# Kernel tuning notes

Hardware: AMD Instinct MI355X
Metric: run time of the kernel (lower is better)

## Reference

```python
import jax, jax.numpy as jnp
import numpy as np

N, DIM, K = 65536, 512, 256


def setup_inputs() -> dict:
    key = jax.random.key(0)
    k1, k2 = jax.random.split(key)
    embeddings = jax.random.normal(k1, (N, DIM), dtype=jnp.float32)
    # Centroid table produced by the (external, non-differentiable) faiss
    # k-means fit; materialized here as a learned parameter.
    centroids = jax.random.normal(k2, (K, DIM), dtype=jnp.float32)
    return {"embeddings": embeddings, "centroids": centroids, "batch_id": 0}


def reference(embeddings, centroids, batch_id):
    # Batched equivalent of the Python loop over samples:
    # for each embedding, cdist to centroids, take the 2nd-nearest centroid.
    # Squared L2 preserves the ordering of torch.cdist (monotone sqrt),
    # and the output is a gather of centroids, so math is identical.
    # d2: [N, K]
    d2 = (
        jnp.sum(embeddings * embeddings, axis=1, keepdims=True)
        - 2.0 * jnp.einsum("nd,kd->nk", embeddings, centroids)
        + jnp.sum(centroids * centroids, axis=1)
    )
    # top-2 smallest distances -> indices of nearest and 2nd-nearest centroids
    _, top2_idx = jax.lax.top_k(-d2, 2)  # [N, 2]
    hard_neg_idx = top2_idx[:, 1]  # second-nearest centroid per sample
    return centroids[hard_neg_idx]  # [N, DIM]
```

## Files before the change

### kernel.cpp

```cpp
#include <hip/hip_runtime.h>

#define N_EMB 65536
#define DIM   512
#define K_C   256
#define NCHUNK (DIM / 32)
#define RPW   16
#define WAVES 4
#define THETA 1.5f


typedef __attribute__((ext_vector_type(4))) float        f32x4;
typedef __attribute__((ext_vector_type(8))) __bf16       bf16x8;
typedef __attribute__((ext_vector_type(8))) short        s16x8;
typedef __attribute__((ext_vector_type(4))) unsigned int u32x4;

template <class T>
__device__ inline auto mfma_bf16_t(T a, T b, f32x4 c, int)
    -> decltype(__builtin_amdgcn_mfma_f32_16x16x32_bf16(a, b, c, 0, 0, 0)) {
  return __builtin_amdgcn_mfma_f32_16x16x32_bf16(a, b, c, 0, 0, 0);
}
template <class T>
__device__ inline f32x4 mfma_bf16_t(T a, T b, f32x4 c, long) {
  return __builtin_amdgcn_mfma_f32_16x16x32_bf16(
      __builtin_bit_cast(s16x8, a), __builtin_bit_cast(s16x8, b), c, 0, 0, 0);
}
__device__ inline f32x4 MFMA(bf16x8 a, bf16x8 b, f32x4 c) {
  return mfma_bf16_t(a, b, c, 0);
}

__device__ inline unsigned umin_(unsigned a, unsigned b) { return a < b ? a : b; }
__device__ inline unsigned umax_(unsigned a, unsigned b) { return a > b ? a : b; }

__device__ inline u32x4 pack8hi(const float4 a, const float4 b) {
  return (u32x4){
      (__float_as_uint(a.x) >> 16) | (__float_as_uint(a.y) & 0xFFFF0000u),
      (__float_as_uint(a.z) >> 16) | (__float_as_uint(a.w) & 0xFFFF0000u),
      (__float_as_uint(b.x) >> 16) | (__float_as_uint(b.y) & 0xFFFF0000u),
      (__float_as_uint(b.z) >> 16) | (__float_as_uint(b.w) & 0xFFFF0000u)};
}

__device__ inline u32x4 cvt8hi_rne(const float4 a, const float4 b) {
  float v[8] = {a.x, a.y, a.z, a.w, b.x, b.y, b.z, b.w};
  unsigned h[8];
#pragma unroll
  for (int i = 0; i < 8; ++i) {
    const unsigned u = __float_as_uint(v[i]);
    h[i] = (u + 0x7FFFu + ((u >> 16) & 1u)) >> 16;
  }
  return (u32x4){h[0] | (h[1] << 16), h[2] | (h[3] << 16),
                 h[4] | (h[5] << 16), h[6] | (h[7] << 16)};
}

__global__ void pack_centroids(const float* __restrict__ cent,
                               unsigned* __restrict__ cbh,
                               float* __restrict__ cnorm) {
  const int k    = blockIdx.x;
  const int lane = threadIdx.x;
  const float* src = cent + (size_t)k * DIM + lane * 8;
  const float4 a = *(const float4*)src;
  const float4 b = *(const float4*)(src + 4);
  const int chunk = lane >> 2, g = lane & 3;
  ((u32x4*)cbh)[((size_t)chunk * 16 + (k >> 4)) * 64 + g * 16 + (k & 15)] =
      cvt8hi_rne(a, b);
  float s = a.x * a.x + a.y * a.y + a.z * a.z + a.w * a.w +
            b.x * b.x + b.y * b.y + b.z * b.z + b.w * b.w;
#pragma unroll
  for (int off = 32; off > 0; off >>= 1) s += __shfl_down(s, off, 64);
  if (lane == 0) cnorm[k] = s;
}

__global__ __launch_bounds__(256, 3)
void neg_sampler_main(const float* __restrict__ emb,
                      const float* __restrict__ cent,
                      const unsigned* __restrict__ cbh,
                      const float* __restrict__ cnorm,
                      float* __restrict__ out) {
  __shared__ unsigned top4s[WAVES][RPW][4];

  const int tid  = threadIdx.x;
  const int lane = tid & 63;
  const int w    = tid >> 6;
  const int row0 = (blockIdx.x * WAVES + w) * RPW;
  const int frow = lane & 15, fgrp = lane >> 4;

  f32x4 acc[16];
#pragma unroll
  for (int j = 0; j < 16; ++j) acc[j] = (f32x4){0.f, 0.f, 0.f, 0.f};

  const float* const ep = emb + (size_t)(row0 + frow) * DIM + fgrp * 8;
  float4 ea = *(const float4*)(ep);
  float4 eb = *(const float4*)(ep + 4);

  const u32x4* const cs = (const u32x4*)cbh + lane;
  u32x4 A[8], B[8];
#pragma unroll
  for (int i = 0; i < 8; ++i) A[i] = cs[i * 64];
#pragma unroll
  for (int i = 0; i < 8; ++i) B[i] = cs[512 + i * 64];

  for (int c = 0; c < NCHUNK; ++c) {
    const int cn = (c + 1) & (NCHUNK - 1);
    const float4 na = *(const float4*)(ep + cn * 32);
    const float4 nb = *(const float4*)(ep + cn * 32 + 4);
    const bf16x8 eh = __builtin_bit_cast(bf16x8, pack8hi(ea, eb));

#pragma unroll
    for (int i = 0; i < 8; ++i)
      acc[i] = MFMA(eh, __builtin_bit_cast(bf16x8, A[i]), acc[i]);
    const u32x4* const csn = cs + (size_t)cn * 1024;
#pragma unroll
    for (int i = 0; i < 8; ++i) A[i] = csn[i * 64];

#pragma unroll
    for (int i = 0; i < 8; ++i)
      acc[8 + i] = MFMA(eh, __builtin_bit_cast(bf16x8, B[i]), acc[8 + i]);
#pragma unroll
    for (int i = 0; i < 8; ++i) B[i] = csn[512 + i * 64];

    ea = na; eb = nb;
  }

  const int lcol = lane & 15, lgrp = lane >> 4;
  float cnv[16];
#pragma unroll
  for (int ct = 0; ct < 16; ++ct) cnv[ct] = cnorm[ct * 16 + lcol];

#pragma unroll
  for (int rg = 0; rg < 4; ++rg) {
    unsigned b0_ = 0xFFFFFFFFu, b1_ = b0_, b2_ = b0_, b3_ = b0_;
    auto ins = [&](unsigned u) {
      b3_ = umin_(b3_, umax_(b2_, u));
      b2_ = umin_(b2_, umax_(b1_, u));
      b1_ = umin_(b1_, umax_(b0_, u));
      b0_ = umin_(b0_, u);
    };
#pragma unroll
    for (int ct = 0; ct < 16; ++ct) {
      const float s = fmaf(-2.f, acc[ct][rg], cnv[ct]);
      ins((__float_as_uint(s) & 0xFFFFFF00u) | (unsigned)(ct * 16 + lcol));
    }
#pragma unroll
    for (int off = 1; off < 16; off <<= 1) {
      const unsigned o0 = __shfl_xor(b0_, off, 64);
      const unsigned o1 = __shfl_xor(b1_, off, 64);
      const unsigned o2 = __shfl_xor(b2_, off, 64);
      const unsigned o3 = __shfl_xor(b3_, off, 64);
      ins(o0); ins(o1); ins(o2); ins(o3);
    }
    if (lcol == 0) {
      const int rl = lgrp * 4 + rg;
      *(u32x4*)&top4s[w][rl][0] = (u32x4){b0_, b1_, b2_, b3_};
    }
  }

  for (int rr = 0; rr < RPW; ++rr) {
    const unsigned u0 = top4s[w][rr][0], u1 = top4s[w][rr][1];
    const unsigned u2 = top4s[w][rr][2], u3 = top4s[w][rr][3];
    const float a0s = __uint_as_float(u0 & 0xFFFFFF00u);
    const float a1s = __uint_as_float(u1 & 0xFFFFFF00u);
    const float a2s = __uint_as_float(u2 & 0xFFFFFF00u);
    int i2;
    if (a1s - a0s >= THETA && a2s - a1s >= THETA) {
      i2 = (int)(u1 & 0xFFu);
    } else {
      const int grow = row0 + rr;
      const int c0 = (int)(u0 & 0xFFu), c1 = (int)(u1 & 0xFFu);
      const int c2 = (int)(u2 & 0xFFu), c3 = (int)(u3 & 0xFFu);

      const float4* e4 = (const float4*)(emb + (size_t)grow * DIM) + lane * 2;
      const float4 ev0 = e4[0], ev1 = e4[1];

      auto pdot = [&](int cj) {
        const float4* c4 = (const float4*)(cent + (size_t)cj * DIM) + lane * 2;
        const float4 cv0 = c4[0], cv1 = c4[1];
        float d = ev0.x * cv0.x;
        d = fmaf(ev0.y, cv0.y, d); d = fmaf(ev0.z, cv0.z, d);
        d = fmaf(ev0.w, cv0.w, d);
        d = fmaf(ev1.x, cv1.x, d); d = fmaf(ev1.y, cv1.y, d);
        d = fmaf(ev1.z, cv1.z, d); d = fmaf(ev1.w, cv1.w, d);
        return d;
      };
      float d0 = pdot(c0), d1 = pdot(c1), d2 = pdot(c2), d3 = pdot(c3);
#pragma unroll
      for (int off = 1; off < 64; off <<= 1) {
        d0 += __shfl_xor(d0, off, 64);
        d1 += __shfl_xor(d1, off, 64);
        d2 += __shfl_xor(d2, off, 64);
        d3 += __shfl_xor(d3, off, 64);
      }
      const float s0 = fmaf(-2.f, d0, cnorm[c0]);
      const float s1 = fmaf(-2.f, d1, cnorm[c1]);
      const float s2 = fmaf(-2.f, d2, cnorm[c2]);
      const float s3 = fmaf(-2.f, d3, cnorm[c3]);

      float v1 = s0, v2 = 3.4e38f;
      int i1 = c0; i2 = K_C;
      auto upd = [&](float s, int ci) {
        if (s < v1 || (s == v1 && ci < i1)) { v2 = v1; i2 = i1; v1 = s; i1 = ci; }
        else if (s < v2 || (s == v2 && ci < i2)) { v2 = s; i2 = ci; }
      };
      upd(s1, c1); upd(s2, c2); upd(s3, c3);
    }
    if (lane == 0) top4s[w][rr][3] = (unsigned)i2;
  }

  unsigned nid = top4s[w][0][3];
  const float4* sp = (const float4*)(cent + (size_t)nid * DIM) + lane * 2;
  float4 g0 = sp[0], g1 = sp[1];
  for (int rr = 0; rr < RPW; ++rr) {
    const float4 o0 = g0, o1 = g1;
    if (rr + 1 < RPW) {
      nid = top4s[w][rr + 1][3];
      sp = (const float4*)(cent + (size_t)nid * DIM) + lane * 2;
      g0 = sp[0]; g1 = sp[1];
    }
    float4* op = (float4*)(out + (size_t)(row0 + rr) * DIM) + lane * 2;
    op[0] = o0;
    op[1] = o1;
  }
}

extern "C" void kernel_launch(void* const* d_in, const int* in_sizes, int n_in,
                              void* d_out, int out_size, void* d_ws, size_t ws_size,
                              hipStream_t stream) {
  (void)in_sizes; (void)n_in; (void)out_size; (void)ws_size;
  const float* emb  = (const float*)d_in[0];
  const float* cent = (const float*)d_in[1];
  unsigned* cbh = (unsigned*)d_ws;
  float* cnorm  = (float*)((char*)d_ws + 256 * 1024);

  pack_centroids<<<K_C, 64, 0, stream>>>(cent, cbh, cnorm);
  neg_sampler_main<<<N_EMB / (WAVES * RPW), 256, 0, stream>>>(emb, cent, cbh,
                                                              cnorm, (float*)d_out);
}
```

Measured before the change: 289.3 us.

## Split centroid columns across wave pairs and stage bf16 embeddings in LDS

Each block now handles 32 rows. The block cooperatively loads the embedding tile, converts it to bf16 and stores it in swizzled shared memory. Each wave pair covers 16 rows, and each wave computes only half of the 256 centroids, so the per-wave accumulator drops from 16 to 8 tiles. The two halves' top-4 lists are merged through LDS before the refine and gather steps. The aim is to cut register pressure, raise occupancy and remove per-wave global embedding loads, at the cost of more blocks, two barriers and centroid fragment loads duplicated across wave pairs.

```diff
diff --git a/kernel.cpp b/kernel.cpp
--- a/kernel.cpp
+++ b/kernel.cpp
@@ -1,12 +1,12 @@
 #include <hip/hip_runtime.h>
 
-#define N_EMB 65536
-#define DIM   512
-#define K_C   256
-#define NCHUNK (DIM / 32)
-#define RPW   16
-#define WAVES 4
-#define THETA 1.5f
+#define N_EMB  65536
+#define DIM    512
+#define K_C    256
+#define NCHUNK 16
+#define ROWS_B 32
+#define THETA  1.5f
+#define LDSMSK 0x7FF0u
 
 
 typedef __attribute__((ext_vector_type(4))) float        f32x4;
@@ -75,55 +75,76 @@
                       const unsigned* __restrict__ cbh,
                       const float* __restrict__ cnorm,
                       float* __restrict__ out) {
-  __shared__ unsigned top4s[WAVES][RPW][4];
+  __shared__ __align__(16) char     ebh[ROWS_B * 1024];
+  __shared__ __align__(16) unsigned qtop[ROWS_B][2][4];
+  __shared__ __align__(16) unsigned ridx[ROWS_B];
 
   const int tid  = threadIdx.x;
   const int lane = tid & 63;
   const int w    = tid >> 6;
-  const int row0 = (blockIdx.x * WAVES + w) * RPW;
-  const int frow = lane & 15, fgrp = lane >> 4;
-
-  f32x4 acc[16];
-#pragma unroll
-  for (int j = 0; j < 16; ++j) acc[j] = (f32x4){0.f, 0.f, 0.f, 0.f};
-
-  const float* const ep = emb + (size_t)(row0 + frow) * DIM + fgrp * 8;
-  float4 ea = *(const float4*)(ep);
-  float4 eb = *(const float4*)(ep + 4);
-
-  const u32x4* const cs = (const u32x4*)cbh + lane;
+  const int h    = w >> 1;
+  const int q    = w & 1;
+  const int row0 = blockIdx.x * ROWS_B;
+
+  {
+    const float* tb = emb + (size_t)row0 * DIM;
+    float4 va[8], vb[8];
+#pragma unroll
+    for (int i = 0; i < 8; ++i) {
+      const float* sp = tb + (size_t)(i * 4 + w) * DIM + lane * 8;
+      va[i] = *(const float4*)sp;
+      vb[i] = *(const float4*)(sp + 4);
+    }
+#pragma unroll
+    for (int i = 0; i < 8; ++i) {
+      const int r = i * 4 + w;
+      const unsigned byte =
+          ((unsigned)(r * 1024 + lane * 16) ^ (unsigned)((r & 7) << 4)) & LDSMSK;
+      *(u32x4*)(ebh + byte) = pack8hi(va[i], vb[i]);
+    }
+  }
+
+  const u32x4* const cs = (const u32x4*)cbh + q * 8 * 64 + lane;
   u32x4 A[8], B[8];
 #pragma unroll
   for (int i = 0; i < 8; ++i) A[i] = cs[i * 64];
 #pragma unroll
-  for (int i = 0; i < 8; ++i) B[i] = cs[512 + i * 64];
-
-  for (int c = 0; c < NCHUNK; ++c) {
-    const int cn = (c + 1) & (NCHUNK - 1);
-    const float4 na = *(const float4*)(ep + cn * 32);
-    const float4 nb = *(const float4*)(ep + cn * 32 + 4);
-    const bf16x8 eh = __builtin_bit_cast(bf16x8, pack8hi(ea, eb));
-
+  for (int i = 0; i < 8; ++i) B[i] = cs[1024 + i * 64];
+
+  __syncthreads();
+
+  f32x4 acc[8];
+#pragma unroll
+  for (int i = 0; i < 8; ++i) acc[i] = (f32x4){0.f, 0.f, 0.f, 0.f};
+
+  const unsigned ebase = (unsigned)(h * 16 * 1024);
+  const unsigned elin  = (unsigned)((lane & 15) * 1024 + (lane >> 4) * 16);
+  const unsigned exr   = (unsigned)((lane & 7) << 4);
+
+  for (int c2 = 0; c2 < NCHUNK; c2 += 2) {
+    const unsigned off0 = (ebase + ((elin + c2 * 64) ^ exr)) & LDSMSK;
+    const bf16x8 eh0 = *(const bf16x8*)(ebh + off0);
 #pragma unroll
     for (int i = 0; i < 8; ++i)
-      acc[i] = MFMA(eh, __builtin_bit_cast(bf16x8, A[i]), acc[i]);
-    const u32x4* const csn = cs + (size_t)cn * 1024;
-#pragma unroll
-    for (int i = 0; i < 8; ++i) A[i] = csn[i * 64];
-
+      acc[i] = MFMA(eh0, __builtin_bit_cast(bf16x8, A[i]), acc[i]);
+    const int ca = (c2 + 2) & 15;
+#pragma unroll
+    for (int i = 0; i < 8; ++i) A[i] = cs[ca * 1024 + i * 64];
+
+    const unsigned off1 = (ebase + ((elin + c2 * 64 + 64) ^ exr)) & LDSMSK;
+    const bf16x8 eh1 = *(const bf16x8*)(ebh + off1);
 #pragma unroll
     for (int i = 0; i < 8; ++i)
-      acc[8 + i] = MFMA(eh, __builtin_bit_cast(bf16x8, B[i]), acc[8 + i]);
-#pragma unroll
-    for (int i = 0; i < 8; ++i) B[i] = csn[512 + i * 64];
-
-    ea = na; eb = nb;
+      acc[i] = MFMA(eh1, __builtin_bit_cast(bf16x8, B[i]), acc[i]);
+    const int cb2 = (c2 + 3) & 15;
+#pragma unroll
+    for (int i = 0; i < 8; ++i) B[i] = cs[cb2 * 1024 + i * 64];
   }
 
   const int lcol = lane & 15, lgrp = lane >> 4;
-  float cnv[16];
-#pragma unroll
-  for (int ct = 0; ct < 16; ++ct) cnv[ct] = cnorm[ct * 16 + lcol];
+  float cnv[8];
+#pragma unroll
+  for (int i = 0; i < 8; ++i) cnv[i] = cnorm[(q * 8 + i) * 16 + lcol];
 
 #pragma unroll
   for (int rg = 0; rg < 4; ++rg) {
@@ -135,9 +156,10 @@
       b0_ = umin_(b0_, u);
     };
 #pragma unroll
-    for (int ct = 0; ct < 16; ++ct) {
-      const float s = fmaf(-2.f, acc[ct][rg], cnv[ct]);
-      ins((__float_as_uint(s) & 0xFFFFFF00u) | (unsigned)(ct * 16 + lcol));
+    for (int i = 0; i < 8; ++i) {
+      const float s = fmaf(-2.f, acc[i][rg], cnv[i]);
+      ins((__float_as_uint(s) & 0xFFFFFF00u) |
+          (unsigned)((q * 8 + i) * 16 + lcol));
     }
 #pragma unroll
     for (int off = 1; off < 16; off <<= 1) {
@@ -148,28 +170,39 @@
       ins(o0); ins(o1); ins(o2); ins(o3);
     }
     if (lcol == 0) {
-      const int rl = lgrp * 4 + rg;
-      *(u32x4*)&top4s[w][rl][0] = (u32x4){b0_, b1_, b2_, b3_};
-    }
-  }
-
-  for (int rr = 0; rr < RPW; ++rr) {
-    const unsigned u0 = top4s[w][rr][0], u1 = top4s[w][rr][1];
-    const unsigned u2 = top4s[w][rr][2], u3 = top4s[w][rr][3];
-    const float a0s = __uint_as_float(u0 & 0xFFFFFF00u);
-    const float a1s = __uint_as_float(u1 & 0xFFFFFF00u);
-    const float a2s = __uint_as_float(u2 & 0xFFFFFF00u);
+      const int row = h * 16 + lgrp * 4 + rg;
+      *(u32x4*)&qtop[row][q][0] = (u32x4){b0_, b1_, b2_, b3_};
+    }
+  }
+
+  __syncthreads();
+
+  for (int rr = 0; rr < 8; ++rr) {
+    const int row  = w * 8 + rr;
+    const int grow = row0 + row;
+    const u32x4 qa = *(const u32x4*)&qtop[row][0][0];
+    const u32x4 qb = *(const u32x4*)&qtop[row][1][0];
+    unsigned m0 = qa[0], m1 = qa[1], m2 = qa[2], m3 = qa[3];
+    auto ins = [&](unsigned u) {
+      m3 = umin_(m3, umax_(m2, u));
+      m2 = umin_(m2, umax_(m1, u));
+      m1 = umin_(m1, umax_(m0, u));
+      m0 = umin_(m0, u);
+    };
+    ins(qb[0]); ins(qb[1]); ins(qb[2]); ins(qb[3]);
+
+    const float a0s = __uint_as_float(m0 & 0xFFFFFF00u);
+    const float a1s = __uint_as_float(m1 & 0xFFFFFF00u);
+    const float a2s = __uint_as_float(m2 & 0xFFFFFF00u);
     int i2;
     if (a1s - a0s >= THETA && a2s - a1s >= THETA) {
-      i2 = (int)(u1 & 0xFFu);
+      i2 = (int)(m1 & 0xFFu);
     } else {
-      const int grow = row0 + rr;
-      const int c0 = (int)(u0 & 0xFFu), c1 = (int)(u1 & 0xFFu);
-      const int c2 = (int)(u2 & 0xFFu), c3 = (int)(u3 & 0xFFu);
+      const int c0 = (int)(m0 & 0xFFu), c1 = (int)(m1 & 0xFFu);
+      const int c2 = (int)(m2 & 0xFFu), c3 = (int)(m3 & 0xFFu);
 
       const float4* e4 = (const float4*)(emb + (size_t)grow * DIM) + lane * 2;
       const float4 ev0 = e4[0], ev1 = e4[1];
-
       auto pdot = [&](int cj) {
         const float4* c4 = (const float4*)(cent + (size_t)cj * DIM) + lane * 2;
         const float4 cv0 = c4[0], cv1 = c4[1];
@@ -201,20 +234,20 @@
       };
       upd(s1, c1); upd(s2, c2); upd(s3, c3);
     }
-    if (lane == 0) top4s[w][rr][3] = (unsigned)i2;
-  }
-
-  unsigned nid = top4s[w][0][3];
+    if (lane == 0) ridx[row] = (unsigned)i2 & 255u;
+  }
+
+  unsigned nid = ridx[w * 8] & 255u;
   const float4* sp = (const float4*)(cent + (size_t)nid * DIM) + lane * 2;
   float4 g0 = sp[0], g1 = sp[1];
-  for (int rr = 0; rr < RPW; ++rr) {
+  for (int rr = 0; rr < 8; ++rr) {
     const float4 o0 = g0, o1 = g1;
-    if (rr + 1 < RPW) {
-      nid = top4s[w][rr + 1][3];
+    if (rr + 1 < 8) {
+      nid = ridx[w * 8 + rr + 1] & 255u;
       sp = (const float4*)(cent + (size_t)nid * DIM) + lane * 2;
       g0 = sp[0]; g1 = sp[1];
     }
-    float4* op = (float4*)(out + (size_t)(row0 + rr) * DIM) + lane * 2;
+    float4* op = (float4*)(out + (size_t)(row0 + w * 8 + rr) * DIM) + lane * 2;
     op[0] = o0;
     op[1] = o1;
   }
@@ -230,6 +263,6 @@
   float* cnorm  = (float*)((char*)d_ws + 256 * 1024);
 
   pack_centroids<<<K_C, 64, 0, stream>>>(cent, cbh, cnorm);
-  neg_sampler_main<<<N_EMB / (WAVES * RPW), 256, 0, stream>>>(emb, cent, cbh,
-                                                              cnorm, (float*)d_out);
-}
+  neg_sampler_main<<<N_EMB / ROWS_B, 256, 0, stream>>>(emb, cent, cbh, cnorm,
+                                                       (float*)d_out);
+}
```

Result: no change. 290.7 us (+0.5%).

## Split centroid gather into a separate kernel and raise select occupancy

Applied to the files above, without the earlier changes.

The fused kernel is split in two. The selection kernel now writes only the chosen centroid index into the first float of each output row, and a new gather kernel reads that index and copies the matching centroid row to the output with coalesced float4 stores. This takes the 128 MB output write out of the register-heavy MFMA kernel, so the launch-bounds occupancy hint is raised from 3 to 4 blocks. In exchange it adds a kernel launch and an extra global round trip for the indices, and it relies on launch ordering on the stream for correctness.

```diff
diff --git a/kernel.cpp b/kernel.cpp
--- a/kernel.cpp
+++ b/kernel.cpp
@@ -1,12 +1,13 @@
 #include <hip/hip_runtime.h>
 
-#define N_EMB 65536
-#define DIM   512
-#define K_C   256
-#define NCHUNK (DIM / 32)
-#define RPW   16
-#define WAVES 4
-#define THETA 1.5f
+
+#define N_EMB  65536
+#define DIM    512
+#define K_C    256
+#define NCHUNK 16
+#define RPW    16
+#define WAVES  4
+#define THETA  1.5f
 
 
 typedef __attribute__((ext_vector_type(4))) float        f32x4;
@@ -69,12 +70,12 @@
   if (lane == 0) cnorm[k] = s;
 }
 
-__global__ __launch_bounds__(256, 3)
-void neg_sampler_main(const float* __restrict__ emb,
-                      const float* __restrict__ cent,
-                      const unsigned* __restrict__ cbh,
-                      const float* __restrict__ cnorm,
-                      float* __restrict__ out) {
+__global__ __launch_bounds__(256, 4)
+void select_kernel(const float* __restrict__ emb,
+                   const float* __restrict__ cent,
+                   const unsigned* __restrict__ cbh,
+                   const float* __restrict__ cnorm,
+                   float* __restrict__ out) {
   __shared__ unsigned top4s[WAVES][RPW][4];
 
   const int tid  = threadIdx.x;
@@ -154,6 +155,7 @@
   }
 
   for (int rr = 0; rr < RPW; ++rr) {
+    const int grow = row0 + rr;
     const unsigned u0 = top4s[w][rr][0], u1 = top4s[w][rr][1];
     const unsigned u2 = top4s[w][rr][2], u3 = top4s[w][rr][3];
     const float a0s = __uint_as_float(u0 & 0xFFFFFF00u);
@@ -163,13 +165,11 @@
     if (a1s - a0s >= THETA && a2s - a1s >= THETA) {
       i2 = (int)(u1 & 0xFFu);
     } else {
-      const int grow = row0 + rr;
       const int c0 = (int)(u0 & 0xFFu), c1 = (int)(u1 & 0xFFu);
       const int c2 = (int)(u2 & 0xFFu), c3 = (int)(u3 & 0xFFu);
 
       const float4* e4 = (const float4*)(emb + (size_t)grow * DIM) + lane * 2;
       const float4 ev0 = e4[0], ev1 = e4[1];
-
       auto pdot = [&](int cj) {
         const float4* c4 = (const float4*)(cent + (size_t)cj * DIM) + lane * 2;
         const float4 cv0 = c4[0], cv1 = c4[1];
@@ -201,22 +201,26 @@
       };
       upd(s1, c1); upd(s2, c2); upd(s3, c3);
     }
-    if (lane == 0) top4s[w][rr][3] = (unsigned)i2;
-  }
-
-  unsigned nid = top4s[w][0][3];
-  const float4* sp = (const float4*)(cent + (size_t)nid * DIM) + lane * 2;
-  float4 g0 = sp[0], g1 = sp[1];
-  for (int rr = 0; rr < RPW; ++rr) {
-    const float4 o0 = g0, o1 = g1;
-    if (rr + 1 < RPW) {
-      nid = top4s[w][rr + 1][3];
-      sp = (const float4*)(cent + (size_t)nid * DIM) + lane * 2;
-      g0 = sp[0]; g1 = sp[1];
-    }
-    float4* op = (float4*)(out + (size_t)(row0 + rr) * DIM) + lane * 2;
-    op[0] = o0;
-    op[1] = o1;
+    if (lane == 0)
+      out[(size_t)grow * DIM] = __uint_as_float((unsigned)i2);
+  }
+}
+
+__global__ __launch_bounds__(256, 8)
+void gather_kernel(const float* __restrict__ cent, float* __restrict__ out) {
+  __shared__ unsigned sidx[8];
+  const int tid = threadIdx.x;
+  const int r0  = blockIdx.x * 8;
+  if (tid < 8)
+    sidx[tid] = __float_as_uint(out[(size_t)(r0 + tid) * DIM]) & 255u;
+  __syncthreads();
+  const float4* c4 = (const float4*)cent;
+  float4* o4 = (float4*)(out + (size_t)r0 * DIM);
+#pragma unroll
+  for (int j = 0; j < 4; ++j) {
+    const int g = j * 256 + tid;
+    const int rrel = g >> 7, off = g & 127;
+    o4[g] = c4[sidx[rrel] * 128 + off];
   }
 }
 
@@ -230,6 +234,7 @@
   float* cnorm  = (float*)((char*)d_ws + 256 * 1024);
 
   pack_centroids<<<K_C, 64, 0, stream>>>(cent, cbh, cnorm);
-  neg_sampler_main<<<N_EMB / (WAVES * RPW), 256, 0, stream>>>(emb, cent, cbh,
-                                                              cnorm, (float*)d_out);
-}
+  select_kernel<<<N_EMB / (WAVES * RPW), 256, 0, stream>>>(emb, cent, cbh, cnorm,
+                                                           (float*)d_out);
+  gather_kernel<<<N_EMB / 8, 256, 0, stream>>>(cent, (float*)d_out);
+}
```

Result: slower. 309.3 us (+6.9%).
